# Optimization experiments

Hardware: AMD Instinct MI355X
Metric: run time of the kernel (lower is better)

Reference implementation:

```python
import jax, jax.numpy as jnp
import numpy as np

B, N, M, C, H, NNZ = 64, 2048, 2048, 64, 128, 32768


def setup_inputs() -> dict:
    key = jax.random.key(0)
    ks = jax.random.split(key, 7)
    x = jax.random.normal(ks[0], (B * N, H), dtype=jnp.float32)
    batch = jnp.repeat(jnp.arange(B, dtype=jnp.int32), N)  # sorted graph ids
    d_rows = jax.random.randint(ks[1], (B, NNZ), 0, M, dtype=jnp.int32)
    d_cols = jax.random.randint(ks[2], (B, NNZ), 0, N, dtype=jnp.int32)
    d_vals = jax.random.normal(ks[3], (B, NNZ), dtype=jnp.float32) * (1.0 / np.sqrt(16.0))
    d_index = jax.random.randint(ks[4], (B, M), 0, C, dtype=jnp.int32)
    w_scale = 1.0 / np.sqrt(3 * H)
    Wq = jax.random.normal(ks[5], (3 * H, H), dtype=jnp.float32) * w_scale
    Wk = jax.random.normal(ks[6], (3 * H, H), dtype=jnp.float32) * w_scale
    Wv = jax.random.normal(jax.random.fold_in(key, 7), (3 * H, H), dtype=jnp.float32) * w_scale
    return {"x": x, "batch": batch, "batch_size": B, "d_rows": d_rows,
            "d_cols": d_cols, "d_vals": d_vals, "d_index": d_index,
            "Wq": Wq, "Wk": Wk, "Wv": Wv}


def _per_graph(xg, rows, cols, vals, idx, Wq, Wk, Wv):
    # spmm: coefs[r] = sum_e vals[e] * xg[cols[e]] for rows[e] == r  -> [M, H]
    coefs = jax.ops.segment_sum(vals[:, None] * xg[cols], rows, num_segments=M)
    # three segment poolings over cluster index -> each [C, H]
    s = jax.ops.segment_sum(coefs, idx, num_segments=C)
    cnt = jax.ops.segment_sum(jnp.ones((M,), coefs.dtype), idx, num_segments=C)
    mean = s / jnp.maximum(cnt, 1.0)[:, None]
    mx = jax.ops.segment_max(coefs, idx, num_segments=C)
    x_dec = jnp.concatenate([mean, mx, s], axis=1)  # [C, 3H]
    # small self-attention over clusters (linear layers without bias)
    Q = x_dec @ Wq
    K = x_dec @ Wk
    V = x_dec @ Wv
    dist = jax.nn.softmax((Q @ K.T) * (1.0 / np.sqrt(H)), axis=-1)
    return (dist @ V).reshape(-1)  # [C*H]


def reference(x, batch, batch_size, d_rows, d_cols, d_vals, d_index, Wq, Wk, Wv):
    # nodes are sorted by graph with equal graph size N, so x[batch==i] == xb[i]
    xb = x.reshape(batch_size, N, H)
    out = jax.vmap(_per_graph, in_axes=(0, 0, 0, 0, 0, None, None, None))(
        xb, d_rows, d_cols, d_vals, d_index, Wq, Wk, Wv)
    return out  # [B, C*H] == torch.vstack of per-graph flattened attentions
```

## Files before the change

### kernel.cpp

```cpp
#include <hip/hip_runtime.h>
#include <hip/hip_fp16.h>

#define BG 64
#define NN 2048
#define MM 2048
#define CC 64
#define HH 128
#define NNZE 32768
#define TH 384

typedef float f4v __attribute__((ext_vector_type(4)));
typedef __attribute__((ext_vector_type(8))) short bf16x8;
typedef __attribute__((ext_vector_type(4))) float f32x4;
typedef unsigned short u16;

static __device__ __forceinline__ u16 bf16rne(float f) {
    uint u = __float_as_uint(f);
    uint r = u + 0x7FFFu + ((u >> 16) & 1u);
    return (u16)(r >> 16);
}
static __device__ __forceinline__ float bf16tof(u16 h) {
    return __uint_as_float(((uint)h) << 16);
}

__global__ __launch_bounds__(1024) void prep_count_kernel(const int* __restrict__ d_rows,
                                                          const int* __restrict__ d_index,
                                                          const float* __restrict__ x,
                                                          const float* __restrict__ Wq,
                                                          const float* __restrict__ Wk,
                                                          const float* __restrict__ Wv,
                                                          int* __restrict__ cnt_blk,
                                                          int* __restrict__ cnt_clu_blk,
                                                          uint* __restrict__ xh,
                                                          u16* __restrict__ WhT,
                                                          u16* __restrict__ WlT) {
    __shared__ int cnt_row_s[MM];
    __shared__ int cnt_clu_s[CC];
    int gb = blockIdx.x;
    int g = gb >> 2, b = gb & 3;
    int t = threadIdx.x;
    cnt_row_s[t] = 0;
    cnt_row_s[t + 1024] = 0;
    if (t < CC) cnt_clu_s[t] = 0;
    __syncthreads();
    const int* rows_g = d_rows + ((size_t)g << 15) + (b << 13);
#pragma unroll
    for (int it = 0; it < 8; it++) atomicAdd(&cnt_row_s[rows_g[it * 1024 + t]], 1);
    if (t < 512) atomicAdd(&cnt_clu_s[d_index[(g << 11) + (b << 9) + t]], 1);

    {
        const f4v* x4 = (const f4v*)x;
        uint4* xh4 = (uint4*)xh;
#pragma unroll
        for (int it = 0; it < 8; it++) {
            int tidg = (gb << 13) + it * 1024 + t;
            f4v a = __builtin_nontemporal_load(&x4[2 * tidg]);
            f4v bb = __builtin_nontemporal_load(&x4[2 * tidg + 1]);
            __half2 h0 = __float22half2_rn(make_float2(a.x, a.y));
            __half2 h1 = __float22half2_rn(make_float2(a.z, a.w));
            __half2 h2 = __float22half2_rn(make_float2(bb.x, bb.y));
            __half2 h3 = __float22half2_rn(make_float2(bb.z, bb.w));
            uint4 o;
            o.x = *(uint*)&h0;
            o.y = *(uint*)&h1;
            o.z = *(uint*)&h2;
            o.w = *(uint*)&h3;
            xh4[tidg] = o;
        }
    }
    if (gb < 144) {
        int id = (gb << 10) + t;
        int w = id / 49152;
        int r = id - w * 49152;
        const float* Ws = (w == 0) ? Wq : (w == 1) ? Wk : Wv;
        float v = Ws[r];
        int k = r >> 7, n = r & 127;
        u16 hi = bf16rne(v);
        u16 lo = bf16rne(v - bf16tof(hi));
        WhT[w * 49152 + n * 384 + k] = hi;
        WlT[w * 49152 + n * 384 + k] = lo;
    }
    __syncthreads();
    int* cb = cnt_blk + (size_t)gb * MM;
    cb[t] = cnt_row_s[t];
    cb[t + 1024] = cnt_row_s[t + 1024];
    if (t < CC) cnt_clu_blk[gb * CC + t] = cnt_clu_s[t];
}

__global__ __launch_bounds__(1024) void prep_scan_kernel(const int* __restrict__ d_index,
                                                         const int* __restrict__ cnt_blk,
                                                         const int* __restrict__ cnt_clu_blk,
                                                         int* __restrict__ cnt_clu_g,
                                                         int* __restrict__ off_clu_g,
                                                         int* __restrict__ row_edge_off_g,
                                                         int* __restrict__ off_row_blk,
                                                         int* __restrict__ end_pos) {
    __shared__ int cnt_clu_s[CC], off_clu_s[CC], fill_clu_s[CC];
    __shared__ int rlist_s[MM];
    __shared__ int rowtot_s[MM];
    __shared__ int blk1_s[MM], blk2_s[MM], blk3_s[MM];
    __shared__ int off_row_s[MM];
    __shared__ int wsum[16];
    int g = blockIdx.x, t = threadIdx.x;
    int lane = t & 63, w = t >> 6;

    const int* cb = cnt_blk + ((size_t)g << 2) * MM;
    for (int r = t; r < MM; r += 1024) {
        int c0 = cb[r], c1 = cb[MM + r], c2 = cb[2 * MM + r], c3 = cb[3 * MM + r];
        blk1_s[r] = c0;
        blk2_s[r] = c0 + c1;
        blk3_s[r] = c0 + c1 + c2;
        rowtot_s[r] = c0 + c1 + c2 + c3;
    }
    if (t < CC) {
        const int* ccb = cnt_clu_blk + (g << 2) * CC;
        int v = ccb[t] + ccb[CC + t] + ccb[2 * CC + t] + ccb[3 * CC + t];
        cnt_clu_s[t] = v;
        fill_clu_s[t] = 0;
        int incl = v;
#pragma unroll
        for (int d = 1; d < 64; d <<= 1) {
            int u = __shfl_up(incl, d);
            if (t >= d) incl += u;
        }
        off_clu_s[t] = incl - v;
        cnt_clu_g[(g << 6) + t] = v;
        off_clu_g[(g << 6) + t] = incl - v;
    }
    int idx0 = d_index[(g << 11) + t];
    int idx1 = d_index[(g << 11) + t + 1024];
    __syncthreads();

    {
        int s0 = atomicAdd(&fill_clu_s[idx0], 1);
        rlist_s[off_clu_s[idx0] + s0] = t;
        int s1 = atomicAdd(&fill_clu_s[idx1], 1);
        rlist_s[off_clu_s[idx1] + s1] = t + 1024;
    }
    __syncthreads();

    int r0 = rlist_s[2 * t], r1 = rlist_s[2 * t + 1];
    int c0 = rowtot_s[r0], c1 = rowtot_s[r1];
    int s = c0 + c1;
    int incl = s;
#pragma unroll
    for (int d = 1; d < 64; d <<= 1) {
        int u = __shfl_up(incl, d);
        if (lane >= d) incl += u;
    }
    if (lane == 63) wsum[w] = incl;
    __syncthreads();
    if (t < 16) {
        int v = wsum[t], iv = v;
#pragma unroll
        for (int d = 1; d < 16; d <<= 1) {
            int u = __shfl_up(iv, d);
            if (t >= d) iv += u;
        }
        wsum[t] = iv - v;
    }
    __syncthreads();
    {
        int base = wsum[w] + incl - s;
        int* reo = row_edge_off_g + g * (MM + 1);
        reo[2 * t] = base;
        reo[2 * t + 1] = base + c0;
        off_row_s[r0] = base;
        off_row_s[r1] = base + c0;
        if (t == 0) reo[MM] = NNZE;
    }
    __syncthreads();

    int* ob = off_row_blk + ((size_t)g << 2) * MM;
    int* epp = end_pos + (size_t)g * MM;
    for (int r = t; r < MM; r += 1024) {
        int orr = off_row_s[r];
        ob[r] = orr;
        ob[MM + r] = orr + blk1_s[r];
        ob[2 * MM + r] = orr + blk2_s[r];
        ob[3 * MM + r] = orr + blk3_s[r];
        epp[r] = orr + rowtot_s[r];
    }
}

__global__ __launch_bounds__(1024) void prep_bin_kernel(const int* __restrict__ d_rows,
                                                        const int* __restrict__ d_cols,
                                                        const float* __restrict__ d_vals,
                                                        const int* __restrict__ off_row_blk,
                                                        const int* __restrict__ end_pos,
                                                        int2* __restrict__ epack) {
    __shared__ int off_s[MM];
    __shared__ int end_s[MM];
    __shared__ int fill_s[MM];
    int gb = blockIdx.x;
    int g = gb >> 2, b = gb & 3;
    int t = threadIdx.x;
    const int* ob = off_row_blk + (size_t)gb * MM;
    const int* epp = end_pos + (size_t)g * MM;
    off_s[t] = ob[t];
    off_s[t + 1024] = ob[t + 1024];
    end_s[t] = epp[t];
    end_s[t + 1024] = epp[t + 1024];
    fill_s[t] = 0;
    fill_s[t + 1024] = 0;
    __syncthreads();
    const int* rows_g = d_rows + ((size_t)g << 15) + (b << 13);
    const int* cols_g = d_cols + ((size_t)g << 15) + (b << 13);
    const float* vals_g = d_vals + ((size_t)g << 15) + (b << 13);
    int2* epg = epack + ((size_t)g << 15);
#pragma unroll
    for (int it = 0; it < 8; it++) {
        int e = it * 1024 + t;
        int r = rows_g[e];
        int slot = atomicAdd(&fill_s[r], 1);
        int pos = off_s[r] + slot;
        int flag = (pos == end_s[r] - 1) ? (int)0x80000000 : 0;
        epg[pos] = make_int2(cols_g[e] | flag, __float_as_int(vals_g[e]));
    }
}

__global__ __launch_bounds__(64) void spmm_pool_kernel(const uint* __restrict__ xh,
                                                       const int* __restrict__ cnt_clu,
                                                       const int* __restrict__ off_clu,
                                                       const int* __restrict__ row_edge_off,
                                                       const int2* __restrict__ epack,
                                                       u16* __restrict__ xdh,
                                                       u16* __restrict__ xdl) {
    int bid = blockIdx.x;
    int l = bid >> 3;
    int g = ((bid & 7) << 3) + (l >> 6);
    int c = l & 63;
    int h = threadIdx.x;
    int gc = (g << 6) + c;
    int rcnt = cnt_clu[gc];
    int j0 = off_clu[gc];
    const int* reo = row_edge_off + g * (MM + 1) + j0;
    int ebase = reo[0];
    int etot = reo[rcnt] - ebase;
    const long long* ep = (const long long*)(epack + ((size_t)g << 15)) + ebase;
    const uint* xg = xh + ((size_t)g << 17);
    float2 coef = make_float2(0.f, 0.f), sum = make_float2(0.f, 0.f);
    float2 mx = make_float2(-__builtin_inff(), -__builtin_inff());
    int e = 0;
    for (; e + 16 <= etot; e += 16) {
        long long q[16];
#pragma unroll
        for (int k = 0; k < 16; k++) q[k] = __builtin_nontemporal_load(&ep[e + k]);
        uint xv[16];
#pragma unroll
        for (int k = 0; k < 16; k++)
            xv[k] = xg[(((uint)(int)q[k] & 0x7FFFFFFFu) << 6) + h];
#pragma unroll
        for (int k = 0; k < 16; k++) {
            float v = __int_as_float((int)(q[k] >> 32));
            float2 f = __half22float2(*(__half2*)&xv[k]);
            coef.x = fmaf(v, f.x, coef.x);
            coef.y = fmaf(v, f.y, coef.y);
            if ((int)q[k] < 0) {
                sum.x += coef.x; sum.y += coef.y;
                mx.x = fmaxf(mx.x, coef.x); mx.y = fmaxf(mx.y, coef.y);
                coef.x = 0.f; coef.y = 0.f;
            }
        }
    }
    for (; e < etot; e++) {
        long long q = ep[e];
        uint xv = xg[(((uint)(int)q & 0x7FFFFFFFu) << 6) + h];
        float v = __int_as_float((int)(q >> 32));
        float2 f = __half22float2(*(__half2*)&xv);
        coef.x = fmaf(v, f.x, coef.x);
        coef.y = fmaf(v, f.y, coef.y);
        if ((int)q < 0) {
            sum.x += coef.x; sum.y += coef.y;
            mx.x = fmaxf(mx.x, coef.x); mx.y = fmaxf(mx.y, coef.y);
            coef.x = 0.f; coef.y = 0.f;
        }
    }
    int az = 0;
    for (int j = h; j < rcnt; j += 64) az |= (reo[j + 1] == reo[j]);
    if (__ballot(az) != 0ULL) {
        mx.x = fmaxf(mx.x, 0.f);
        mx.y = fmaxf(mx.y, 0.f);
    }
    float inv = 1.f / (float)(rcnt > 0 ? rcnt : 1);
    uint* oh = (uint*)xdh + (size_t)gc * 192 + h;
    uint* ol = (uint*)xdl + (size_t)gc * 192 + h;
    float me0 = sum.x * inv, me1 = sum.y * inv;
    u16 a0 = bf16rne(me0), a1 = bf16rne(me1);
    oh[0] = (uint)a0 | ((uint)a1 << 16);
    ol[0] = (uint)bf16rne(me0 - bf16tof(a0)) | ((uint)bf16rne(me1 - bf16tof(a1)) << 16);
    u16 b0 = bf16rne(mx.x), b1 = bf16rne(mx.y);
    oh[64] = (uint)b0 | ((uint)b1 << 16);
    ol[64] = (uint)bf16rne(mx.x - bf16tof(b0)) | ((uint)bf16rne(mx.y - bf16tof(b1)) << 16);
    u16 c0 = bf16rne(sum.x), c1 = bf16rne(sum.y);
    oh[128] = (uint)c0 | ((uint)c1 << 16);
    ol[128] = (uint)bf16rne(sum.x - bf16tof(c0)) | ((uint)bf16rne(sum.y - bf16tof(c1)) << 16);
}

__global__ __launch_bounds__(256) void qkv_kernel(const u16* __restrict__ xdh,
                                                  const u16* __restrict__ xdl,
                                                  const u16* __restrict__ WhT,
                                                  const u16* __restrict__ WlT,
                                                  float* __restrict__ QKV) {
    __shared__ u16 Ah[64][40], Al[64][40], Bh[64][40], Bl[64][40];
    int bx = blockIdx.x, by = blockIdx.y;
    int t = threadIdx.x;
    int w = by >> 1;
    int cb = (by & 1) << 6;
    int r0 = bx << 6;
    const u16* wh = WhT + w * 49152;
    const u16* wl = WlT + w * 49152;
    int lane = t & 63, wv = t >> 6;
    int wm = wv >> 1, wn = wv & 1;
    int srow = t >> 2, sks = (t & 3) << 3;
    int fr = lane & 15, fk = (lane >> 4) << 3;
    f32x4 acc[2][2];
#pragma unroll
    for (int i = 0; i < 2; i++)
#pragma unroll
        for (int j = 0; j < 2; j++)
#pragma unroll
            for (int r = 0; r < 4; r++) acc[i][j][r] = 0.f;
    for (int ks = 0; ks < 12; ks++) {
        int k0 = ks << 5;
        bf16x8 sa_h = *(const bf16x8*)&xdh[(size_t)(r0 + srow) * 384 + k0 + sks];
        bf16x8 sa_l = *(const bf16x8*)&xdl[(size_t)(r0 + srow) * 384 + k0 + sks];
        bf16x8 sb_h = *(const bf16x8*)&wh[(size_t)(cb + srow) * 384 + k0 + sks];
        bf16x8 sb_l = *(const bf16x8*)&wl[(size_t)(cb + srow) * 384 + k0 + sks];
        if (ks) __syncthreads();
        *(bf16x8*)&Ah[srow][sks] = sa_h;
        *(bf16x8*)&Al[srow][sks] = sa_l;
        *(bf16x8*)&Bh[srow][sks] = sb_h;
        *(bf16x8*)&Bl[srow][sks] = sb_l;
        __syncthreads();
        bf16x8 fa_h[2], fa_l[2], fb_h[2], fb_l[2];
#pragma unroll
        for (int mi = 0; mi < 2; mi++) {
            int ar = (wm << 5) + (mi << 4) + fr;
            fa_h[mi] = *(const bf16x8*)&Ah[ar][fk];
            fa_l[mi] = *(const bf16x8*)&Al[ar][fk];
        }
#pragma unroll
        for (int ni = 0; ni < 2; ni++) {
            int br = (wn << 5) + (ni << 4) + fr;
            fb_h[ni] = *(const bf16x8*)&Bh[br][fk];
            fb_l[ni] = *(const bf16x8*)&Bl[br][fk];
        }
#pragma unroll
        for (int mi = 0; mi < 2; mi++)
#pragma unroll
            for (int ni = 0; ni < 2; ni++) {
                acc[mi][ni] = __builtin_amdgcn_mfma_f32_16x16x32_bf16(
                    fa_h[mi], fb_h[ni], acc[mi][ni], 0, 0, 0);
                acc[mi][ni] = __builtin_amdgcn_mfma_f32_16x16x32_bf16(
                    fa_h[mi], fb_l[ni], acc[mi][ni], 0, 0, 0);
                acc[mi][ni] = __builtin_amdgcn_mfma_f32_16x16x32_bf16(
                    fa_l[mi], fb_h[ni], acc[mi][ni], 0, 0, 0);
            }
    }
#pragma unroll
    for (int mi = 0; mi < 2; mi++)
#pragma unroll
        for (int ni = 0; ni < 2; ni++)
#pragma unroll
            for (int r = 0; r < 4; r++) {
                int row = r0 + (wm << 5) + (mi << 4) + ((lane >> 4) << 2) + r;
                int col = (by << 6) + (wn << 5) + (ni << 4) + (lane & 15);
                QKV[(size_t)row * TH + col] = acc[mi][ni][r];
            }
}

__global__ __launch_bounds__(256) void attn_kernel(const float* __restrict__ QKV,
                                                   float* __restrict__ out) {
    __shared__ float Qs[16][132];
    __shared__ float sc[16][68];
    int g = blockIdx.x;
    int q0 = blockIdx.y * 16;
    int t = threadIdx.x;
    const float* base = QKV + (size_t)(g * CC) * TH;
    for (int u = t; u < 512; u += 256) {
        int i = u >> 5, cc = u & 31;
        *(float4*)&Qs[i][cc * 4] = *(const float4*)&base[(size_t)(q0 + i) * TH + cc * 4];
    }
    __syncthreads();
    {
        int j = t & 63, iq = t >> 6;
        float a0 = 0, a1 = 0, a2 = 0, a3 = 0;
        const float* Krow = base + (size_t)j * TH + HH;
#pragma unroll 4
        for (int cc = 0; cc < 32; cc++) {
            float4 kv = *(const float4*)&Krow[cc * 4];
            float4 q0v = *(float4*)&Qs[iq][cc * 4];
            float4 q1v = *(float4*)&Qs[4 + iq][cc * 4];
            float4 q2v = *(float4*)&Qs[8 + iq][cc * 4];
            float4 q3v = *(float4*)&Qs[12 + iq][cc * 4];
            a0 += kv.x * q0v.x + kv.y * q0v.y + kv.z * q0v.z + kv.w * q0v.w;
            a1 += kv.x * q1v.x + kv.y * q1v.y + kv.z * q1v.z + kv.w * q1v.w;
            a2 += kv.x * q2v.x + kv.y * q2v.y + kv.z * q2v.z + kv.w * q2v.w;
            a3 += kv.x * q3v.x + kv.y * q3v.y + kv.z * q3v.z + kv.w * q3v.w;
        }
        const float scale = 0.08838834764831845f;
        sc[iq][j] = a0 * scale;
        sc[4 + iq][j] = a1 * scale;
        sc[8 + iq][j] = a2 * scale;
        sc[12 + iq][j] = a3 * scale;
    }
    __syncthreads();
    {
        int i = t >> 4, l = t & 15;
        float4 sv = *(float4*)&sc[i][l * 4];
        float m = fmaxf(fmaxf(sv.x, sv.y), fmaxf(sv.z, sv.w));
#pragma unroll
        for (int d = 1; d < 16; d <<= 1) m = fmaxf(m, __shfl_xor(m, d));
        float4 p;
        p.x = __expf(sv.x - m);
        p.y = __expf(sv.y - m);
        p.z = __expf(sv.z - m);
        p.w = __expf(sv.w - m);
        float s = p.x + p.y + p.z + p.w;
#pragma unroll
        for (int d = 1; d < 16; d <<= 1) s += __shfl_xor(s, d);
        float inv = 1.0f / s;
        p.x *= inv; p.y *= inv; p.z *= inv; p.w *= inv;
        *(float4*)&sc[i][l * 4] = p;
    }
    __syncthreads();
    {
        int i = t >> 4, hq = t & 15;
        const float* Vbase = base + 2 * HH;
        float acc[8] = {};
        for (int j = 0; j < 64; j++) {
            float d = sc[i][j];
            float4 v0 = *(const float4*)&Vbase[(size_t)j * TH + hq * 8];
            float4 v1 = *(const float4*)&Vbase[(size_t)j * TH + hq * 8 + 4];
            acc[0] = fmaf(d, v0.x, acc[0]);
            acc[1] = fmaf(d, v0.y, acc[1]);
            acc[2] = fmaf(d, v0.z, acc[2]);
            acc[3] = fmaf(d, v0.w, acc[3]);
            acc[4] = fmaf(d, v1.x, acc[4]);
            acc[5] = fmaf(d, v1.y, acc[5]);
            acc[6] = fmaf(d, v1.z, acc[6]);
            acc[7] = fmaf(d, v1.w, acc[7]);
        }
        float* op = out + (size_t)g * (CC * HH) + (size_t)(q0 + i) * HH + hq * 8;
        *(float4*)&op[0] = make_float4(acc[0], acc[1], acc[2], acc[3]);
        *(float4*)&op[4] = make_float4(acc[4], acc[5], acc[6], acc[7]);
    }
}

extern "C" void kernel_launch(void* const* d_in, const int* in_sizes, int n_in,
                              void* d_out, int out_size, void* d_ws, size_t ws_size,
                              hipStream_t stream) {
    const float* x = (const float*)d_in[0];
    const int* d_rows = (const int*)d_in[3];
    const int* d_cols = (const int*)d_in[4];
    const float* d_vals = (const float*)d_in[5];
    const int* d_index = (const int*)d_in[6];
    const float* Wq = (const float*)d_in[7];
    const float* Wk = (const float*)d_in[8];
    const float* Wv = (const float*)d_in[9];
    float* out = (float*)d_out;

    char* ws = (char*)d_ws;
    size_t o = 0;
    uint* xh = (uint*)(ws + o); o += (size_t)BG * NN * (HH / 2) * 4;
    int2* epack = (int2*)(ws + o); o += (size_t)BG * NNZE * 8;
    int* cnt_blk = (int*)(ws + o); o += (size_t)BG * 4 * MM * 4;
    int* off_row_blk = (int*)(ws + o); o += (size_t)BG * 4 * MM * 4;
    int* end_pos = (int*)(ws + o); o += (size_t)BG * MM * 4;
    int* cnt_clu_blk = (int*)(ws + o); o += (size_t)BG * 4 * CC * 4;
    int* row_edge_off = (int*)(ws + o); o += (size_t)BG * (MM + 1) * 4;
    int* cnt_clu = (int*)(ws + o); o += (size_t)BG * CC * 4;
    int* off_clu = (int*)(ws + o); o += (size_t)BG * CC * 4;
    u16* xdh = (u16*)(ws + o); o += (size_t)BG * CC * TH * 2;
    u16* xdl = (u16*)(ws + o); o += (size_t)BG * CC * TH * 2;
    u16* WhT = (u16*)(ws + o); o += (size_t)3 * HH * TH * 2;
    u16* WlT = (u16*)(ws + o); o += (size_t)3 * HH * TH * 2;
    float* QKV = (float*)(ws + o); o += (size_t)BG * CC * TH * 4;

    prep_count_kernel<<<BG * 4, 1024, 0, stream>>>(d_rows, d_index, x, Wq, Wk, Wv,
                                                   cnt_blk, cnt_clu_blk, xh, WhT, WlT);
    prep_scan_kernel<<<BG, 1024, 0, stream>>>(d_index, cnt_blk, cnt_clu_blk,
                                              cnt_clu, off_clu, row_edge_off,
                                              off_row_blk, end_pos);
    prep_bin_kernel<<<BG * 4, 1024, 0, stream>>>(d_rows, d_cols, d_vals,
                                                 off_row_blk, end_pos, epack);
    spmm_pool_kernel<<<BG * CC, 64, 0, stream>>>(xh, cnt_clu, off_clu, row_edge_off,
                                                 epack, xdh, xdl);
    qkv_kernel<<<dim3(64, 6), 256, 0, stream>>>(xdh, xdl, WhT, WlT, QKV);
    attn_kernel<<<dim3(BG, 4), 256, 0, stream>>>(QKV, out);
}
```

Before: 258.0 us.

## Fuse count, scan and bin preprocessing into one per-graph kernel

Merges the three preprocessing kernels (row counting, offset scan, edge binning) plus the x half-conversion and weight split into a single kernel with one 1024-thread block per graph. Per-block count and offset arrays now stay in shared memory, which removes their global round trips and two kernel launches. Index loads are widened to int4. In exchange, parallelism drops from 256 blocks to 64 blocks, and each block serially handles 32K edges and 256K x elements, which can leave many CUs idle on a large GPU.

```diff
diff --git a/kernel.cpp b/kernel.cpp
--- a/kernel.cpp
+++ b/kernel.cpp
@@ -23,100 +23,51 @@
     return __uint_as_float(((uint)h) << 16);
 }
 
-__global__ __launch_bounds__(1024) void prep_count_kernel(const int* __restrict__ d_rows,
-                                                          const int* __restrict__ d_index,
-                                                          const float* __restrict__ x,
-                                                          const float* __restrict__ Wq,
-                                                          const float* __restrict__ Wk,
-                                                          const float* __restrict__ Wv,
-                                                          int* __restrict__ cnt_blk,
-                                                          int* __restrict__ cnt_clu_blk,
-                                                          uint* __restrict__ xh,
-                                                          u16* __restrict__ WhT,
-                                                          u16* __restrict__ WlT) {
+__global__ __launch_bounds__(1024) void prep_all_kernel(
+    const int* __restrict__ d_rows, const int* __restrict__ d_cols,
+    const float* __restrict__ d_vals, const int* __restrict__ d_index,
+    const float* __restrict__ x,
+    const float* __restrict__ Wq, const float* __restrict__ Wk,
+    const float* __restrict__ Wv,
+    uint* __restrict__ xh, u16* __restrict__ WhT, u16* __restrict__ WlT,
+    int* __restrict__ cnt_clu_g, int* __restrict__ off_clu_g,
+    int* __restrict__ row_edge_off_g, int2* __restrict__ epack) {
     __shared__ int cnt_row_s[MM];
-    __shared__ int cnt_clu_s[CC];
-    int gb = blockIdx.x;
-    int g = gb >> 2, b = gb & 3;
-    int t = threadIdx.x;
-    cnt_row_s[t] = 0;
-    cnt_row_s[t + 1024] = 0;
-    if (t < CC) cnt_clu_s[t] = 0;
-    __syncthreads();
-    const int* rows_g = d_rows + ((size_t)g << 15) + (b << 13);
-#pragma unroll
-    for (int it = 0; it < 8; it++) atomicAdd(&cnt_row_s[rows_g[it * 1024 + t]], 1);
-    if (t < 512) atomicAdd(&cnt_clu_s[d_index[(g << 11) + (b << 9) + t]], 1);
-
-    {
-        const f4v* x4 = (const f4v*)x;
-        uint4* xh4 = (uint4*)xh;
-#pragma unroll
-        for (int it = 0; it < 8; it++) {
-            int tidg = (gb << 13) + it * 1024 + t;
-            f4v a = __builtin_nontemporal_load(&x4[2 * tidg]);
-            f4v bb = __builtin_nontemporal_load(&x4[2 * tidg + 1]);
-            __half2 h0 = __float22half2_rn(make_float2(a.x, a.y));
-            __half2 h1 = __float22half2_rn(make_float2(a.z, a.w));
-            __half2 h2 = __float22half2_rn(make_float2(bb.x, bb.y));
-            __half2 h3 = __float22half2_rn(make_float2(bb.z, bb.w));
-            uint4 o;
-            o.x = *(uint*)&h0;
-            o.y = *(uint*)&h1;
-            o.z = *(uint*)&h2;
-            o.w = *(uint*)&h3;
-            xh4[tidg] = o;
-        }
-    }
-    if (gb < 144) {
-        int id = (gb << 10) + t;
-        int w = id / 49152;
-        int r = id - w * 49152;
-        const float* Ws = (w == 0) ? Wq : (w == 1) ? Wk : Wv;
-        float v = Ws[r];
-        int k = r >> 7, n = r & 127;
-        u16 hi = bf16rne(v);
-        u16 lo = bf16rne(v - bf16tof(hi));
-        WhT[w * 49152 + n * 384 + k] = hi;
-        WlT[w * 49152 + n * 384 + k] = lo;
-    }
-    __syncthreads();
-    int* cb = cnt_blk + (size_t)gb * MM;
-    cb[t] = cnt_row_s[t];
-    cb[t + 1024] = cnt_row_s[t + 1024];
-    if (t < CC) cnt_clu_blk[gb * CC + t] = cnt_clu_s[t];
-}
-
-__global__ __launch_bounds__(1024) void prep_scan_kernel(const int* __restrict__ d_index,
-                                                         const int* __restrict__ cnt_blk,
-                                                         const int* __restrict__ cnt_clu_blk,
-                                                         int* __restrict__ cnt_clu_g,
-                                                         int* __restrict__ off_clu_g,
-                                                         int* __restrict__ row_edge_off_g,
-                                                         int* __restrict__ off_row_blk,
-                                                         int* __restrict__ end_pos) {
+    __shared__ int off_row_s[MM];
+    __shared__ int fill_s[MM];
+    __shared__ int rlist_s[MM];
     __shared__ int cnt_clu_s[CC], off_clu_s[CC], fill_clu_s[CC];
-    __shared__ int rlist_s[MM];
-    __shared__ int rowtot_s[MM];
-    __shared__ int blk1_s[MM], blk2_s[MM], blk3_s[MM];
-    __shared__ int off_row_s[MM];
     __shared__ int wsum[16];
     int g = blockIdx.x, t = threadIdx.x;
     int lane = t & 63, w = t >> 6;
 
-    const int* cb = cnt_blk + ((size_t)g << 2) * MM;
-    for (int r = t; r < MM; r += 1024) {
-        int c0 = cb[r], c1 = cb[MM + r], c2 = cb[2 * MM + r], c3 = cb[3 * MM + r];
-        blk1_s[r] = c0;
-        blk2_s[r] = c0 + c1;
-        blk3_s[r] = c0 + c1 + c2;
-        rowtot_s[r] = c0 + c1 + c2 + c3;
-    }
+    cnt_row_s[t] = 0;
+    cnt_row_s[t + 1024] = 0;
+    fill_s[t] = 0;
+    fill_s[t + 1024] = 0;
     if (t < CC) {
-        const int* ccb = cnt_clu_blk + (g << 2) * CC;
-        int v = ccb[t] + ccb[CC + t] + ccb[2 * CC + t] + ccb[3 * CC + t];
-        cnt_clu_s[t] = v;
+        cnt_clu_s[t] = 0;
         fill_clu_s[t] = 0;
+    }
+    int idx0 = d_index[(g << 11) + t];
+    int idx1 = d_index[(g << 11) + t + 1024];
+    __syncthreads();
+
+    const int4* rows4 = (const int4*)(d_rows + ((size_t)g << 15));
+#pragma unroll
+    for (int it = 0; it < 8; it++) {
+        int4 r = rows4[it * 1024 + t];
+        atomicAdd(&cnt_row_s[r.x], 1);
+        atomicAdd(&cnt_row_s[r.y], 1);
+        atomicAdd(&cnt_row_s[r.z], 1);
+        atomicAdd(&cnt_row_s[r.w], 1);
+    }
+    atomicAdd(&cnt_clu_s[idx0], 1);
+    atomicAdd(&cnt_clu_s[idx1], 1);
+    __syncthreads();
+
+    if (t < CC) {
+        int v = cnt_clu_s[t];
         int incl = v;
 #pragma unroll
         for (int d = 1; d < 64; d <<= 1) {
@@ -127,8 +78,6 @@
         cnt_clu_g[(g << 6) + t] = v;
         off_clu_g[(g << 6) + t] = incl - v;
     }
-    int idx0 = d_index[(g << 11) + t];
-    int idx1 = d_index[(g << 11) + t + 1024];
     __syncthreads();
 
     {
@@ -140,7 +89,7 @@
     __syncthreads();
 
     int r0 = rlist_s[2 * t], r1 = rlist_s[2 * t + 1];
-    int c0 = rowtot_s[r0], c1 = rowtot_s[r1];
+    int c0 = cnt_row_s[r0], c1 = cnt_row_s[r1];
     int s = c0 + c1;
     int incl = s;
 #pragma unroll
@@ -171,51 +120,67 @@
     }
     __syncthreads();
 
-    int* ob = off_row_blk + ((size_t)g << 2) * MM;
-    int* epp = end_pos + (size_t)g * MM;
-    for (int r = t; r < MM; r += 1024) {
-        int orr = off_row_s[r];
-        ob[r] = orr;
-        ob[MM + r] = orr + blk1_s[r];
-        ob[2 * MM + r] = orr + blk2_s[r];
-        ob[3 * MM + r] = orr + blk3_s[r];
-        epp[r] = orr + rowtot_s[r];
-    }
-}
-
-__global__ __launch_bounds__(1024) void prep_bin_kernel(const int* __restrict__ d_rows,
-                                                        const int* __restrict__ d_cols,
-                                                        const float* __restrict__ d_vals,
-                                                        const int* __restrict__ off_row_blk,
-                                                        const int* __restrict__ end_pos,
-                                                        int2* __restrict__ epack) {
-    __shared__ int off_s[MM];
-    __shared__ int end_s[MM];
-    __shared__ int fill_s[MM];
-    int gb = blockIdx.x;
-    int g = gb >> 2, b = gb & 3;
-    int t = threadIdx.x;
-    const int* ob = off_row_blk + (size_t)gb * MM;
-    const int* epp = end_pos + (size_t)g * MM;
-    off_s[t] = ob[t];
-    off_s[t + 1024] = ob[t + 1024];
-    end_s[t] = epp[t];
-    end_s[t + 1024] = epp[t + 1024];
-    fill_s[t] = 0;
-    fill_s[t + 1024] = 0;
-    __syncthreads();
-    const int* rows_g = d_rows + ((size_t)g << 15) + (b << 13);
-    const int* cols_g = d_cols + ((size_t)g << 15) + (b << 13);
-    const float* vals_g = d_vals + ((size_t)g << 15) + (b << 13);
+    const int4* cols4 = (const int4*)(d_cols + ((size_t)g << 15));
+    const f4v* vals4 = (const f4v*)(d_vals + ((size_t)g << 15));
     int2* epg = epack + ((size_t)g << 15);
 #pragma unroll
     for (int it = 0; it < 8; it++) {
-        int e = it * 1024 + t;
-        int r = rows_g[e];
-        int slot = atomicAdd(&fill_s[r], 1);
-        int pos = off_s[r] + slot;
-        int flag = (pos == end_s[r] - 1) ? (int)0x80000000 : 0;
-        epg[pos] = make_int2(cols_g[e] | flag, __float_as_int(vals_g[e]));
+        int4 r = rows4[it * 1024 + t];
+        int4 c = cols4[it * 1024 + t];
+        f4v v = vals4[it * 1024 + t];
+        {
+            int sl = atomicAdd(&fill_s[r.x], 1);
+            int flag = (sl == cnt_row_s[r.x] - 1) ? (int)0x80000000 : 0;
+            epg[off_row_s[r.x] + sl] = make_int2(c.x | flag, __float_as_int(v.x));
+        }
+        {
+            int sl = atomicAdd(&fill_s[r.y], 1);
+            int flag = (sl == cnt_row_s[r.y] - 1) ? (int)0x80000000 : 0;
+            epg[off_row_s[r.y] + sl] = make_int2(c.y | flag, __float_as_int(v.y));
+        }
+        {
+            int sl = atomicAdd(&fill_s[r.z], 1);
+            int flag = (sl == cnt_row_s[r.z] - 1) ? (int)0x80000000 : 0;
+            epg[off_row_s[r.z] + sl] = make_int2(c.z | flag, __float_as_int(v.z));
+        }
+        {
+            int sl = atomicAdd(&fill_s[r.w], 1);
+            int flag = (sl == cnt_row_s[r.w] - 1) ? (int)0x80000000 : 0;
+            epg[off_row_s[r.w] + sl] = make_int2(c.w | flag, __float_as_int(v.w));
+        }
+    }
+
+    {
+        const f4v* x4 = (const f4v*)(x + ((size_t)g << 18));
+        uint4* xh4 = (uint4*)(xh + ((size_t)g << 17));
+#pragma unroll 4
+        for (int it = 0; it < 32; it++) {
+            int gi = it * 1024 + t;
+            f4v a = __builtin_nontemporal_load(&x4[2 * gi]);
+            f4v b = __builtin_nontemporal_load(&x4[2 * gi + 1]);
+            __half2 h0 = __float22half2_rn(make_float2(a.x, a.y));
+            __half2 h1 = __float22half2_rn(make_float2(a.z, a.w));
+            __half2 h2 = __float22half2_rn(make_float2(b.x, b.y));
+            __half2 h3 = __float22half2_rn(make_float2(b.z, b.w));
+            uint4 o;
+            o.x = *(uint*)&h0;
+            o.y = *(uint*)&h1;
+            o.z = *(uint*)&h2;
+            o.w = *(uint*)&h3;
+            xh4[gi] = o;
+        }
+    }
+    for (int i = t; i < 2304; i += 1024) {
+        int id = g * 2304 + i;
+        int wsel = id / 49152;
+        int r = id - wsel * 49152;
+        const float* Ws = (wsel == 0) ? Wq : (wsel == 1) ? Wk : Wv;
+        float v = Ws[r];
+        int k = r >> 7, n = r & 127;
+        u16 hi = bf16rne(v);
+        u16 lo = bf16rne(v - bf16tof(hi));
+        WhT[wsel * 49152 + n * 384 + k] = hi;
+        WlT[wsel * 49152 + n * 384 + k] = lo;
     }
 }
 
@@ -465,10 +430,6 @@
     size_t o = 0;
     uint* xh = (uint*)(ws + o); o += (size_t)BG * NN * (HH / 2) * 4;
     int2* epack = (int2*)(ws + o); o += (size_t)BG * NNZE * 8;
-    int* cnt_blk = (int*)(ws + o); o += (size_t)BG * 4 * MM * 4;
-    int* off_row_blk = (int*)(ws + o); o += (size_t)BG * 4 * MM * 4;
-    int* end_pos = (int*)(ws + o); o += (size_t)BG * MM * 4;
-    int* cnt_clu_blk = (int*)(ws + o); o += (size_t)BG * 4 * CC * 4;
     int* row_edge_off = (int*)(ws + o); o += (size_t)BG * (MM + 1) * 4;
     int* cnt_clu = (int*)(ws + o); o += (size_t)BG * CC * 4;
     int* off_clu = (int*)(ws + o); o += (size_t)BG * CC * 4;
@@ -478,13 +439,9 @@
     u16* WlT = (u16*)(ws + o); o += (size_t)3 * HH * TH * 2;
     float* QKV = (float*)(ws + o); o += (size_t)BG * CC * TH * 4;
 
-    prep_count_kernel<<<BG * 4, 1024, 0, stream>>>(d_rows, d_index, x, Wq, Wk, Wv,
-                                                   cnt_blk, cnt_clu_blk, xh, WhT, WlT);
-    prep_scan_kernel<<<BG, 1024, 0, stream>>>(d_index, cnt_blk, cnt_clu_blk,
-                                              cnt_clu, off_clu, row_edge_off,
-                                              off_row_blk, end_pos);
-    prep_bin_kernel<<<BG * 4, 1024, 0, stream>>>(d_rows, d_cols, d_vals,
-                                                 off_row_blk, end_pos, epack);
+    prep_all_kernel<<<BG, 1024, 0, stream>>>(d_rows, d_cols, d_vals, d_index, x,
+                                             Wq, Wk, Wv, xh, WhT, WlT,
+                                             cnt_clu, off_clu, row_edge_off, epack);
     spmm_pool_kernel<<<BG * CC, 64, 0, stream>>>(xh, cnt_clu, off_clu, row_edge_off,
                                                  epack, xdh, xdl);
     qkv_kernel<<<dim3(64, 6), 256, 0, stream>>>(xdh, xdl, WhT, WlT, QKV);
```

New measurement: 309.2 us. +19.9%, slower.
